# Optimization experiments

Hardware: AMD Instinct MI355X
Metric: run time of the kernel (lower is better)

The kernel has to match this reference:

```python
import jax, jax.numpy as jnp
import numpy as np

NSPINS = 2  # spin_split = 2 (equal split of the electron axis)


def _rolled_concat(arrays, n, axis=-1):
    """Concatenate list starting at index n, wrapping around (cyclic equivariance)."""
    return jnp.concatenate(arrays[n:] + arrays[:n], axis=axis)


def setup_inputs() -> dict:
    key = jax.random.key(0)
    ks = jax.random.split(key, 5)
    B, N, D1, D2, ND = 4096, 16, 256, 32, 256
    in_1e = jax.random.normal(ks[0], (B, N, D1), jnp.float32)
    in_2e = jax.random.normal(ks[1], (B, N, N, D2), jnp.float32)
    W_unmixed = jax.random.normal(ks[2], (D1, ND), jnp.float32) / np.float32(np.sqrt(D1))
    b_unmixed = jnp.zeros((ND,), jnp.float32)
    W_mixed = jax.random.normal(ks[3], (NSPINS * D1, ND), jnp.float32) / np.float32(np.sqrt(NSPINS * D1))
    W_2e = jax.random.normal(ks[4], (NSPINS * D2, ND), jnp.float32) / np.float32(np.sqrt(NSPINS * D2))
    return {"in_1e": in_1e, "in_2e": in_2e, "W_unmixed": W_unmixed,
            "b_unmixed": b_unmixed, "W_mixed": W_mixed, "W_2e": W_2e}


def reference(in_1e, in_2e, W_unmixed, b_unmixed, W_mixed, W_2e):
    # 1) unmixed: per-particle dense on the 1e stream, then split per spin
    dense_unmixed = in_1e @ W_unmixed + b_unmixed          # (B, N, ND)
    split_unmixed = jnp.split(dense_unmixed, NSPINS, axis=-2)

    # 2) mixed: per-spin means of 1e stream, cyclic concat, shared dense
    split_1e = jnp.split(in_1e, NSPINS, axis=-2)
    split_means = [jnp.mean(s, axis=-2, keepdims=True) for s in split_1e]  # [i: (B,1,D1)]
    split_concat = [_rolled_concat(split_means, i) for i in range(NSPINS)]  # [i: (B,1,NSPINS*D1)]
    all_spins = jnp.concatenate(split_concat, axis=-2)      # (B, NSPINS, NSPINS*D1)
    dense_mixed = all_spins @ W_mixed                       # (B, NSPINS, ND)
    dense_mixed_split = jnp.split(dense_mixed, NSPINS, axis=-2)  # [i: (B,1,ND)]

    # 3) 2e: split row-spin, mean over column-spin blocks, cyclic concat, dense
    split_2e = jnp.split(in_2e, NSPINS, axis=-3)            # [i: (B, n_i, N, D2)]
    concat_2e = []
    for spin in range(NSPINS):
        parts = jnp.split(split_2e[spin], NSPINS, axis=-2)  # [j: (B, n_i, n_j, D2)]
        means = [jnp.mean(p, axis=-2) for p in parts]       # [j: (B, n_i, D2)]
        concat_2e.append(_rolled_concat(means, spin))       # (B, n_i, NSPINS*D2)
    all_2e = jnp.concatenate(concat_2e, axis=-2)            # (B, N, NSPINS*D2)
    dense_2e = all_2e @ W_2e                                # (B, N, ND)
    dense_2e_split = jnp.split(dense_2e, NSPINS, axis=-2)

    # sum per spin (mixed broadcasts over particle dim), concat, activate, skip
    out_splits = [u + m + t for u, m, t in zip(split_unmixed, dense_mixed_split, dense_2e_split)]
    dense_out = jnp.concatenate(out_splits, axis=-2)        # (B, N, ND)
    nonlinear_out = jnp.tanh(dense_out)
    return nonlinear_out + in_1e  # skip connection (D1 == ND)
```

## Files before the change

kernel.cpp:

```cpp
#include <hip/hip_runtime.h>
#include <hip/hip_bf16.h>

typedef __bf16 v8bf16 __attribute__((ext_vector_type(8)));
typedef float f32x4 __attribute__((ext_vector_type(4)));
typedef ushort ushort8_t __attribute__((ext_vector_type(8)));

#define NROW  16
#define D1    256

__device__ __forceinline__ ushort bf16_rne(float x) {
    unsigned u = __builtin_bit_cast(unsigned, x);
    unsigned r = u + 0x7FFFu + ((u >> 16) & 1u);
    return (ushort)(r >> 16);
}
__device__ __forceinline__ float bf16_to_f(ushort h) {
    unsigned u = ((unsigned)h) << 16;
    return __builtin_bit_cast(float, u);
}
__device__ __forceinline__ void split_hi_lo(float x, ushort& hi, ushort& lo) {
    hi = bf16_rne(x);
    float rem = x - bf16_to_f(hi);
    lo = bf16_rne(rem);
}
__device__ __forceinline__ float tanh_fast(float x) {
    float xc = fminf(15.f, fmaxf(-15.f, x));
    float e = __expf(2.f * xc);
    return (e - 1.f) / (e + 1.f);
}

__global__ __launch_bounds__(256) void wtrans(const float* __restrict__ Wu,
                                              const float* __restrict__ W2,
                                              const float* __restrict__ Wm,
                                              ushort* __restrict__ Wthi, ushort* __restrict__ Wtlo,
                                              ushort* __restrict__ Wmthi, ushort* __restrict__ Wmtlo) {
    int t = threadIdx.x;
    int bid = blockIdx.x;
    if (bid < 320) {
        int k = bid;
        float w = (k < 256) ? Wu[k * 256 + t] : W2[(k - 256) * 256 + t];
        ushort hi, lo; split_hi_lo(w, hi, lo);
        Wthi[t * 320 + k] = hi;
        Wtlo[t * 320 + k] = lo;
    } else {
        int k = bid - 320;
        float w = Wm[k * 256 + t];
        ushort hi, lo; split_hi_lo(w, hi, lo);
        Wmthi[t * 512 + k] = hi;
        Wmtlo[t * 512 + k] = lo;
    }
}

__global__ __launch_bounds__(256) void prep1(const float* __restrict__ in1e,
                                             const float* __restrict__ in2e,
                                             ushort* __restrict__ mhi, ushort* __restrict__ mlo,
                                             ushort* __restrict__ t2hi, ushort* __restrict__ t2lo) {
    __shared__ float4 red[4][64];
    int b = blockIdx.x;
    int t = threadIdx.x;
    const float4* in1e4 = (const float4*)in1e;
    const float4* in2e4 = (const float4*)in2e;

    {
        int d4 = t & 7, ch = (t >> 3) & 1, r = t >> 4;
        size_t base4 = ((size_t)(b * 16 + r) * 16 + ch * 8) * 8 + d4;
        float4 s = in2e4[base4];
#pragma unroll
        for (int c = 1; c < 8; c++) {
            float4 v = in2e4[base4 + (size_t)c * 8];
            s.x += v.x; s.y += v.y; s.z += v.z; s.w += v.w;
        }
        s.x *= 0.125f; s.y *= 0.125f; s.z *= 0.125f; s.w *= 0.125f;
        int off = ((ch ^ (r >> 3)) << 5) + d4 * 4;
        size_t dst = (size_t)(b * 16 + r) * 64 + off;
        ushort4 hv, lv;
        split_hi_lo(s.x, hv.x, lv.x); split_hi_lo(s.y, hv.y, lv.y);
        split_hi_lo(s.z, hv.z, lv.z); split_hi_lo(s.w, hv.w, lv.w);
        *(ushort4*)(t2hi + dst) = hv;
        *(ushort4*)(t2lo + dst) = lv;
    }

    {
        int col4 = t & 63, q = t >> 6;
        size_t base4 = (size_t)(b * 16 + q * 4) * 64 + col4;
        float4 s = in1e4[base4];
#pragma unroll
        for (int r = 1; r < 4; r++) {
            float4 v = in1e4[base4 + (size_t)r * 64];
            s.x += v.x; s.y += v.y; s.z += v.z; s.w += v.w;
        }
        red[q][col4] = s;
    }
    __syncthreads();
    if (t < 128) {
        int col4 = t & 63, half = t >> 6;
        float4 a = red[half * 2][col4], c = red[half * 2 + 1][col4];
        float4 m;
        m.x = (a.x + c.x) * 0.125f; m.y = (a.y + c.y) * 0.125f;
        m.z = (a.z + c.z) * 0.125f; m.w = (a.w + c.w) * 0.125f;
        ushort4 hv, lv;
        split_hi_lo(m.x, hv.x, lv.x); split_hi_lo(m.y, hv.y, lv.y);
        split_hi_lo(m.z, hv.z, lv.z); split_hi_lo(m.w, hv.w, lv.w);
        size_t dst = (size_t)b * 512 + half * 256 + col4 * 4;
        *(ushort4*)(mhi + dst) = hv;
        *(ushort4*)(mlo + dst) = lv;
    }
}

__global__ __launch_bounds__(256) void prep2(const ushort* __restrict__ mhi,
                                             const ushort* __restrict__ mlo,
                                             const ushort* __restrict__ Wmthi,
                                             const ushort* __restrict__ Wmtlo,
                                             const float* __restrict__ bias,
                                             float* __restrict__ mixed) {
    __shared__ __align__(16) ushort Amh[32 * 512];
    __shared__ __align__(16) ushort Aml[32 * 512];
    int t = threadIdx.x;
    int lane = t & 63, w = t >> 6;
    int b0 = blockIdx.x * 16;

#pragma unroll
    for (int i = 0; i < 16; i++) {
        int idx = i * 256 + t;
        int off16 = idx & 31;
        int seg = idx >> 5;
        int arr = seg >> 6;
        int rs = seg & 63;
        int row = rs >> 1, half = rs & 1;
        const ushort* src = (arr ? mlo : mhi) +
            (size_t)(b0 + (row >> 1)) * 512 + ((row & 1) ^ half) * 256 + off16 * 8;
        ushort8_t v = *(const ushort8_t*)src;
        unsigned byte = (unsigned)(row * 1024 + half * 512 + off16 * 16);
        byte ^= (unsigned)((row & 7) << 4);
        *(ushort8_t*)((char*)(arr ? Aml : Amh) + byte) = v;
    }
    __syncthreads();

    f32x4 acc[2][4] = {};
    int lrow = lane & 15, lg = lane >> 4;

    for (int ks = 0; ks < 16; ks++) {
        int k = ks * 32 + lg * 8;
        v8bf16 ah[2], al[2];
#pragma unroll
        for (int rf = 0; rf < 2; rf++) {
            int row = rf * 16 + lrow;
            unsigned byte = (unsigned)(row * 1024 + k * 2) ^ (unsigned)((row & 7) << 4);
            ah[rf] = *(const v8bf16*)((char*)Amh + byte);
            al[rf] = *(const v8bf16*)((char*)Aml + byte);
        }
#pragma unroll
        for (int cf = 0; cf < 4; cf++) {
            int col = w * 64 + cf * 16 + lrow;
            v8bf16 bh = *(const v8bf16*)(Wmthi + (size_t)col * 512 + k);
            v8bf16 bl = *(const v8bf16*)(Wmtlo + (size_t)col * 512 + k);
#pragma unroll
            for (int rf = 0; rf < 2; rf++) {
                acc[rf][cf] = __builtin_amdgcn_mfma_f32_16x16x32_bf16(ah[rf], bh, acc[rf][cf], 0, 0, 0);
                acc[rf][cf] = __builtin_amdgcn_mfma_f32_16x16x32_bf16(ah[rf], bl, acc[rf][cf], 0, 0, 0);
                acc[rf][cf] = __builtin_amdgcn_mfma_f32_16x16x32_bf16(al[rf], bh, acc[rf][cf], 0, 0, 0);
            }
        }
    }

#pragma unroll
    for (int rf = 0; rf < 2; rf++) {
#pragma unroll
        for (int cf = 0; cf < 4; cf++) {
            int col = w * 64 + cf * 16 + lrow;
            float bs = bias[col];
#pragma unroll
            for (int r = 0; r < 4; r++) {
                int row = rf * 16 + lg * 4 + r;
                int bl_ = row >> 1, s = row & 1;
                mixed[((size_t)(b0 + bl_) * 2 + s) * 256 + col] = acc[rf][cf][r] + bs;
            }
        }
    }
}

__global__ __launch_bounds__(256) void main_gemm(const float* __restrict__ in1e,
                                                 const ushort* __restrict__ t2hi,
                                                 const ushort* __restrict__ t2lo,
                                                 const ushort* __restrict__ Wthi,
                                                 const ushort* __restrict__ Wtlo,
                                                 const float* __restrict__ mixed,
                                                 float* __restrict__ out) {
    __shared__ __align__(16) ushort Ahi[64 * 320];
    __shared__ __align__(16) ushort Alo[64 * 320];
    int t = threadIdx.x;
    int lane = t & 63, w = t >> 6;
    size_t row0 = (size_t)blockIdx.x * 64;

#pragma unroll
    for (int i = 0; i < 16; i++) {
        int idx = i * 256 + t;
        int row = idx >> 6, c4 = idx & 63;
        float4 v = *(const float4*)(in1e + (row0 + row) * 256 + c4 * 4);
        ushort4 hv, lv;
        split_hi_lo(v.x, hv.x, lv.x); split_hi_lo(v.y, hv.y, lv.y);
        split_hi_lo(v.z, hv.z, lv.z); split_hi_lo(v.w, hv.w, lv.w);
        unsigned byte = (unsigned)(row * 640 + c4 * 8);
        byte ^= (unsigned)((row & 7) << 4);
        *(ushort4*)((char*)Ahi + byte) = hv;
        *(ushort4*)((char*)Alo + byte) = lv;
    }
#pragma unroll
    for (int i = 0; i < 4; i++) {
        int idx = i * 256 + t;
        int row = idx >> 4, c4 = idx & 15;
        ushort4 hv = *(const ushort4*)(t2hi + (row0 + row) * 64 + c4 * 4);
        ushort4 lv = *(const ushort4*)(t2lo + (row0 + row) * 64 + c4 * 4);
        unsigned byte = (unsigned)(row * 640 + 512 + c4 * 8);
        byte ^= (unsigned)((row & 7) << 4);
        *(ushort4*)((char*)Ahi + byte) = hv;
        *(ushort4*)((char*)Alo + byte) = lv;
    }
    __syncthreads();

    f32x4 acc[4][4] = {};
    int lrow = lane & 15, lg = lane >> 4;

    for (int ks = 0; ks < 10; ks++) {
        int kk = ks * 32;
        v8bf16 ah[4], al[4];
#pragma unroll
        for (int rf = 0; rf < 4; rf++) {
            int row = rf * 16 + lrow;
            unsigned byte = (unsigned)(row * 640 + (kk + lg * 8) * 2);
            byte ^= (unsigned)((row & 7) << 4);
            ah[rf] = *(const v8bf16*)((char*)Ahi + byte);
            al[rf] = *(const v8bf16*)((char*)Alo + byte);
        }
#pragma unroll
        for (int cf = 0; cf < 4; cf++) {
            int col = w * 64 + cf * 16 + lrow;
            v8bf16 bh = *(const v8bf16*)(Wthi + (size_t)col * 320 + kk + lg * 8);
            v8bf16 bl = *(const v8bf16*)(Wtlo + (size_t)col * 320 + kk + lg * 8);
#pragma unroll
            for (int rf = 0; rf < 4; rf++) {
                acc[rf][cf] = __builtin_amdgcn_mfma_f32_16x16x32_bf16(ah[rf], bh, acc[rf][cf], 0, 0, 0);
                acc[rf][cf] = __builtin_amdgcn_mfma_f32_16x16x32_bf16(ah[rf], bl, acc[rf][cf], 0, 0, 0);
                acc[rf][cf] = __builtin_amdgcn_mfma_f32_16x16x32_bf16(al[rf], bh, acc[rf][cf], 0, 0, 0);
            }
        }
    }

#pragma unroll
    for (int rf = 0; rf < 4; rf++) {
        size_t bI = (row0 + rf * 16) >> 4;
        int s = lg >> 1;
#pragma unroll
        for (int cf = 0; cf < 4; cf++) {
            int col = w * 64 + cf * 16 + lrow;
            float mx = mixed[(bI * 2 + s) * 256 + col];
            f32x4 a = acc[rf][cf];
#pragma unroll
            for (int r = 0; r < 4; r++) {
                int row = rf * 16 + lg * 4 + r;
                unsigned byte = (unsigned)(row * 640 + col * 2) ^ (unsigned)((row & 7) << 4);
                float rec = bf16_to_f(*(const ushort*)((const char*)Ahi + byte)) +
                            bf16_to_f(*(const ushort*)((const char*)Alo + byte));
                float pre = a[r] + mx;
                out[(row0 + row) * 256 + col] = tanh_fast(pre) + rec;
            }
        }
    }
}

extern "C" void kernel_launch(void* const* d_in, const int* in_sizes, int n_in,
                              void* d_out, int out_size, void* d_ws, size_t ws_size,
                              hipStream_t stream) {
    const float* in1e = (const float*)d_in[0];
    const float* in2e = (const float*)d_in[1];
    const float* Wu   = (const float*)d_in[2];
    const float* bu   = (const float*)d_in[3];
    const float* Wm   = (const float*)d_in[4];
    const float* W2   = (const float*)d_in[5];

    char* ws = (char*)d_ws;
    ushort* t2hi  = (ushort*)(ws);
    ushort* t2lo  = (ushort*)(ws + 8388608);
    ushort* mhi   = (ushort*)(ws + 16777216);
    ushort* mlo   = (ushort*)(ws + 20971520);
    float*  mixed = (float*)(ws + 25165824);
    ushort* Wthi  = (ushort*)(ws + 33554432);
    ushort* Wtlo  = (ushort*)(ws + 33718272);
    ushort* Wmthi = (ushort*)(ws + 33882112);
    ushort* Wmtlo = (ushort*)(ws + 34144256);
    float* out = (float*)d_out;

    wtrans<<<dim3(832), dim3(256), 0, stream>>>(Wu, W2, Wm, Wthi, Wtlo, Wmthi, Wmtlo);
    prep1<<<dim3(4096), dim3(256), 0, stream>>>(in1e, in2e, mhi, mlo, t2hi, t2lo);
    prep2<<<dim3(256), dim3(256), 0, stream>>>(mhi, mlo, Wmthi, Wmtlo, bu, mixed);
    main_gemm<<<dim3(1024), dim3(256), 0, stream>>>(in1e, t2hi, t2lo, Wthi, Wtlo, mixed, out);
}
```

Baseline: 352.4 us.

## Fuse weight conversion into prep kernel and pre-swizzle weights into MFMA fragment layout

Merges the weight hi/lo split kernel into the first prep kernel as extra blocks, removing one launch. The split weights are stored in MFMA B-fragment order, so each lane in the GEMMs reads a contiguous 16-byte chunk and the wave's loads coalesce, replacing per-column strided reads. The tanh epilogue swaps a divide for a hardware reciprocal. The weight blocks now share a grid with the large reduction blocks, and the reciprocal is slightly less exact.

Result: faster. 335.1 us (-4.9%).

```diff
diff --git a/kernel.cpp b/kernel.cpp
--- a/kernel.cpp
+++ b/kernel.cpp
@@ -4,9 +4,6 @@
 typedef __bf16 v8bf16 __attribute__((ext_vector_type(8)));
 typedef float f32x4 __attribute__((ext_vector_type(4)));
 typedef ushort ushort8_t __attribute__((ext_vector_type(8)));
-
-#define NROW  16
-#define D1    256
 
 __device__ __forceinline__ ushort bf16_rne(float x) {
     unsigned u = __builtin_bit_cast(unsigned, x);
@@ -25,38 +22,44 @@
 __device__ __forceinline__ float tanh_fast(float x) {
     float xc = fminf(15.f, fmaxf(-15.f, x));
     float e = __expf(2.f * xc);
-    return (e - 1.f) / (e + 1.f);
-}
-
-__global__ __launch_bounds__(256) void wtrans(const float* __restrict__ Wu,
-                                              const float* __restrict__ W2,
-                                              const float* __restrict__ Wm,
-                                              ushort* __restrict__ Wthi, ushort* __restrict__ Wtlo,
-                                              ushort* __restrict__ Wmthi, ushort* __restrict__ Wmtlo) {
+    return 1.f - 2.f * __builtin_amdgcn_rcpf(e + 1.f);
+}
+
+__global__ __launch_bounds__(256) void prep(const float* __restrict__ in1e,
+                                            const float* __restrict__ in2e,
+                                            const float* __restrict__ Wu,
+                                            const float* __restrict__ W2,
+                                            const float* __restrict__ Wm,
+                                            ushort* __restrict__ mhi, ushort* __restrict__ mlo,
+                                            ushort* __restrict__ t2hi, ushort* __restrict__ t2lo,
+                                            ushort* __restrict__ Wbhi, ushort* __restrict__ Wblo,
+                                            ushort* __restrict__ Wmbhi, ushort* __restrict__ Wmblo) {
+    __shared__ float4 red[4][64];
+    int bid = blockIdx.x;
     int t = threadIdx.x;
-    int bid = blockIdx.x;
-    if (bid < 320) {
-        int k = bid;
-        float w = (k < 256) ? Wu[k * 256 + t] : W2[(k - 256) * 256 + t];
+
+    if (bid >= 4096) {
+        int k; const float* src; ushort* dhi; ushort* dlo;
+        if (bid < 4416) {
+            k = bid - 4096;
+            src = (k < 256) ? (Wu + k * 256) : (W2 + (k - 256) * 256);
+            dhi = Wbhi; dlo = Wblo;
+        } else {
+            k = bid - 4416;
+            src = Wm + k * 256;
+            dhi = Wmbhi; dlo = Wmblo;
+        }
+        int ks = k >> 5, lg = (k >> 3) & 3, e = k & 7;
+        float w = src[t];
+        int cb = t >> 4, lrow = t & 15;
+        int idx = (ks * 16 + cb) * 512 + (lg * 16 + lrow) * 8 + e;
         ushort hi, lo; split_hi_lo(w, hi, lo);
-        Wthi[t * 320 + k] = hi;
-        Wtlo[t * 320 + k] = lo;
-    } else {
-        int k = bid - 320;
-        float w = Wm[k * 256 + t];
-        ushort hi, lo; split_hi_lo(w, hi, lo);
-        Wmthi[t * 512 + k] = hi;
-        Wmtlo[t * 512 + k] = lo;
-    }
-}
-
-__global__ __launch_bounds__(256) void prep1(const float* __restrict__ in1e,
-                                             const float* __restrict__ in2e,
-                                             ushort* __restrict__ mhi, ushort* __restrict__ mlo,
-                                             ushort* __restrict__ t2hi, ushort* __restrict__ t2lo) {
-    __shared__ float4 red[4][64];
-    int b = blockIdx.x;
-    int t = threadIdx.x;
+        dhi[idx] = hi;
+        dlo[idx] = lo;
+        return;
+    }
+
+    int b = bid;
     const float4* in1e4 = (const float4*)in1e;
     const float4* in2e4 = (const float4*)in2e;
 
@@ -108,8 +111,8 @@
 
 __global__ __launch_bounds__(256) void prep2(const ushort* __restrict__ mhi,
                                              const ushort* __restrict__ mlo,
-                                             const ushort* __restrict__ Wmthi,
-                                             const ushort* __restrict__ Wmtlo,
+                                             const ushort* __restrict__ Wmbhi,
+                                             const ushort* __restrict__ Wmblo,
                                              const float* __restrict__ bias,
                                              float* __restrict__ mixed) {
     __shared__ __align__(16) ushort Amh[32 * 512];
@@ -150,9 +153,9 @@
         }
 #pragma unroll
         for (int cf = 0; cf < 4; cf++) {
-            int col = w * 64 + cf * 16 + lrow;
-            v8bf16 bh = *(const v8bf16*)(Wmthi + (size_t)col * 512 + k);
-            v8bf16 bl = *(const v8bf16*)(Wmtlo + (size_t)col * 512 + k);
+            int bidx = (ks * 16 + w * 4 + cf) * 512 + lane * 8;
+            v8bf16 bh = *(const v8bf16*)(Wmbhi + bidx);
+            v8bf16 bl = *(const v8bf16*)(Wmblo + bidx);
 #pragma unroll
             for (int rf = 0; rf < 2; rf++) {
                 acc[rf][cf] = __builtin_amdgcn_mfma_f32_16x16x32_bf16(ah[rf], bh, acc[rf][cf], 0, 0, 0);
@@ -181,8 +184,8 @@
 __global__ __launch_bounds__(256) void main_gemm(const float* __restrict__ in1e,
                                                  const ushort* __restrict__ t2hi,
                                                  const ushort* __restrict__ t2lo,
-                                                 const ushort* __restrict__ Wthi,
-                                                 const ushort* __restrict__ Wtlo,
+                                                 const ushort* __restrict__ Wbhi,
+                                                 const ushort* __restrict__ Wblo,
                                                  const float* __restrict__ mixed,
                                                  float* __restrict__ out) {
     __shared__ __align__(16) ushort Ahi[64 * 320];
@@ -233,9 +236,9 @@
         }
 #pragma unroll
         for (int cf = 0; cf < 4; cf++) {
-            int col = w * 64 + cf * 16 + lrow;
-            v8bf16 bh = *(const v8bf16*)(Wthi + (size_t)col * 320 + kk + lg * 8);
-            v8bf16 bl = *(const v8bf16*)(Wtlo + (size_t)col * 320 + kk + lg * 8);
+            int bidx = (ks * 16 + w * 4 + cf) * 512 + lane * 8;
+            v8bf16 bh = *(const v8bf16*)(Wbhi + bidx);
+            v8bf16 bl = *(const v8bf16*)(Wblo + bidx);
 #pragma unroll
             for (int rf = 0; rf < 4; rf++) {
                 acc[rf][cf] = __builtin_amdgcn_mfma_f32_16x16x32_bf16(ah[rf], bh, acc[rf][cf], 0, 0, 0);
@@ -283,14 +286,15 @@
     ushort* mhi   = (ushort*)(ws + 16777216);
     ushort* mlo   = (ushort*)(ws + 20971520);
     float*  mixed = (float*)(ws + 25165824);
-    ushort* Wthi  = (ushort*)(ws + 33554432);
-    ushort* Wtlo  = (ushort*)(ws + 33718272);
-    ushort* Wmthi = (ushort*)(ws + 33882112);
-    ushort* Wmtlo = (ushort*)(ws + 34144256);
+    ushort* Wbhi  = (ushort*)(ws + 33554432);
+    ushort* Wblo  = (ushort*)(ws + 33718272);
+    ushort* Wmbhi = (ushort*)(ws + 33882112);
+    ushort* Wmblo = (ushort*)(ws + 34144256);
     float* out = (float*)d_out;
 
-    wtrans<<<dim3(832), dim3(256), 0, stream>>>(Wu, W2, Wm, Wthi, Wtlo, Wmthi, Wmtlo);
-    prep1<<<dim3(4096), dim3(256), 0, stream>>>(in1e, in2e, mhi, mlo, t2hi, t2lo);
-    prep2<<<dim3(256), dim3(256), 0, stream>>>(mhi, mlo, Wmthi, Wmtlo, bu, mixed);
-    main_gemm<<<dim3(1024), dim3(256), 0, stream>>>(in1e, t2hi, t2lo, Wthi, Wtlo, mixed, out);
-}
+    prep<<<dim3(4928), dim3(256), 0, stream>>>(in1e, in2e, Wu, W2, Wm,
+                                               mhi, mlo, t2hi, t2lo,
+                                               Wbhi, Wblo, Wmbhi, Wmblo);
+    prep2<<<dim3(256), dim3(256), 0, stream>>>(mhi, mlo, Wmbhi, Wmblo, bu, mixed);
+    main_gemm<<<dim3(1024), dim3(256), 0, stream>>>(in1e, t2hi, t2lo, Wbhi, Wblo, mixed, out);
+}
```
